# Optimization experiments

Hardware: AMD Instinct MI355X
Metric: run time of the kernel (lower is better)

The kernel has to match this reference:

```python
import jax, jax.numpy as jnp
import numpy as np

HIDDEN = 1024
HEADS = 16
HEAD_DIM = HIDDEN // HEADS
ROTARY_PCT = 0.25
ROTARY_DIM = int(HEAD_DIM * ROTARY_PCT)  # 16
BASE = 10000.0
SCALE = HEAD_DIM ** -0.5
EPS = 1e-8


def _rotate_half(x):
    h = x.shape[-1] // 2
    return jnp.concatenate([-x[..., h:], x[..., :h]], axis=-1)


def _apply_rope(q, k, position_ids):
    # q, k: [B, H, S, D]; NeoX-style partial rotary on first ROTARY_DIM dims
    inv_freq = 1.0 / (BASE ** (jnp.arange(0, ROTARY_DIM, 2, dtype=jnp.float32) / ROTARY_DIM))
    freqs = position_ids.astype(jnp.float32)[:, None] * inv_freq[None, :]  # [S, rd/2]
    emb = jnp.concatenate([freqs, freqs], axis=-1)  # [S, rd]
    cos = jnp.cos(emb)[None, None, :, :]
    sin = jnp.sin(emb)[None, None, :, :]

    def rot(x):
        x_rot, x_pass = x[..., :ROTARY_DIM], x[..., ROTARY_DIM:]
        x_rot = x_rot * cos + _rotate_half(x_rot) * sin
        return jnp.concatenate([x_rot, x_pass], axis=-1)

    return rot(q), rot(k)


def _ka_scan(attn_weights, value):
    # attn_weights: [B, H, S, S] causal softmax; value: [B, H, S, D]
    # A[0] = V[0]; A[i] = renorm(attn_weights[i, :i]) @ A[:i]
    S = value.shape[2]
    idx = jnp.arange(S)

    def step(a_buf, i):
        w = attn_weights[:, :, i, :]                      # [B, H, S]
        w = jnp.where(idx[None, None, :] < i, w, 0.0)     # strict past only
        w = w / (jnp.sum(w, axis=-1, keepdims=True) + EPS)
        a_i = jnp.einsum('bhs,bhsd->bhd', w, a_buf)
        a_i = jnp.where(i == 0, value[:, :, 0, :], a_i)
        a_buf = jax.lax.dynamic_update_slice(a_buf, a_i[:, :, None, :], (0, 0, i, 0))
        return a_buf, None

    a_buf, _ = jax.lax.scan(step, jnp.zeros_like(value), jnp.arange(S))
    return a_buf


def setup_inputs() -> dict:
    key = jax.random.key(0)
    k1, k2, k3 = jax.random.split(key, 3)
    B, S = 2, 2048
    hidden_states = jax.random.normal(k1, (B, S, HIDDEN), dtype=jnp.float32)
    position_ids = jnp.arange(S, dtype=jnp.int32)
    Wqkv = jax.random.normal(k2, (HIDDEN, 3 * HIDDEN), dtype=jnp.float32) / np.sqrt(HIDDEN)
    bqkv = jnp.zeros((3 * HIDDEN,), dtype=jnp.float32)
    Wd = jax.random.normal(k3, (HIDDEN, HIDDEN), dtype=jnp.float32) / np.sqrt(HIDDEN)
    bd = jnp.zeros((HIDDEN,), dtype=jnp.float32)
    return {"hidden_states": hidden_states, "position_ids": position_ids,
            "Wqkv": Wqkv, "bqkv": bqkv, "Wd": Wd, "bd": bd}


def reference(hidden_states, position_ids, Wqkv, bqkv, Wd, bd):
    B, S, _ = hidden_states.shape
    qkv = hidden_states @ Wqkv + bqkv                       # [B, S, 3*hidden]
    qkv = qkv.reshape(B, S, 3, HEADS, HEAD_DIM).transpose(2, 0, 3, 1, 4)
    query, key, value = qkv[0], qkv[1], qkv[2]              # [B, H, S, D]
    query, key = _apply_rope(query, key, position_ids)

    scores = jnp.einsum('bhqd,bhkd->bhqk', query, key) * SCALE
    causal = jnp.tril(jnp.ones((S, S), dtype=bool))
    scores = jnp.where(causal[None, None], scores, -jnp.inf)
    attn_weights = jax.nn.softmax(scores, axis=-1)          # [B, H, S, S]

    attn_output = _ka_scan(attn_weights, value)             # [B, H, S, D]
    attn_output = attn_output.transpose(0, 2, 1, 3).reshape(B, S, HIDDEN)
    return attn_output @ Wd + bd
```

## Files before the change

### kernel.cpp

```cpp
#include <hip/hip_runtime.h>

#define S_ 2048
#define EPSF 1e-8f
#define SCALEF 0.125f

typedef short bf16x8 __attribute__((ext_vector_type(8)));
typedef float f32x4 __attribute__((ext_vector_type(4)));

__device__ __forceinline__ unsigned short f2bf(float f){
  unsigned int u = __float_as_uint(f);
  u = (u + 0x7fffu + ((u >> 16) & 1u)) >> 16;
  return (unsigned short)u;
}
__device__ __forceinline__ float bf2f(unsigned short h){
  return __uint_as_float(((unsigned int)h) << 16);
}
__device__ __forceinline__ unsigned short f2bf_trunc(float f){
  return (unsigned short)(__float_as_uint(f) >> 16);
}

#define GLD16(g, l) __builtin_amdgcn_global_load_lds( \
    (const __attribute__((address_space(1))) unsigned int*)(g), \
    (__attribute__((address_space(3))) unsigned int*)(l), 16, 0, 0)

__global__ void k_prep(const float* __restrict__ hs, const float* __restrict__ Wqkv,
                       const float* __restrict__ bqkv, const float* __restrict__ Wd,
                       unsigned short* __restrict__ Ab,
                       unsigned short* __restrict__ WT,
                       float* __restrict__ U){
  __shared__ float t[32][33];
  __shared__ float red[4][64];
  __shared__ float vsh[64];
  int bid = blockIdx.x;
  if (bid < 4096){
    int i = (bid * 256 + threadIdx.x) * 4;
    float4 v = *(const float4*)(hs + i);
    ushort4 o; o.x=f2bf(v.x); o.y=f2bf(v.y); o.z=f2bf(v.z); o.w=f2bf(v.w);
    *(ushort4*)(Ab + i) = o;
  } else if (bid < 6144){
    int q = bid - 4096;
    int nt = q & 63, kt = q >> 6;
    int tx = threadIdx.x & 31, ty = threadIdx.x >> 5;
    #pragma unroll
    for (int r = 0; r < 32; r += 8)
      t[ty + r][tx] = Wqkv[(size_t)(kt*32 + ty + r)*3072 + nt*32 + tx];
    __syncthreads();
    #pragma unroll
    for (int r = 0; r < 32; r += 8)
      WT[(size_t)(nt*32 + ty + r)*1024 + kt*32 + tx] = f2bf(t[tx][ty + r]);
  } else {
    int bh = bid - 6144; int b = bh >> 4, h = bh & 15;
    int d = threadIdx.x & 63, kc = threadIdx.x >> 6;
    const float* x = hs + (size_t)b * S_ * 1024;
    int col = 2048 + h*64 + d;
    float acc = 0.f;
    #pragma unroll 8
    for (int k = kc*256; k < kc*256 + 256; ++k)
      acc = fmaf(x[k], Wqkv[(size_t)k*3072 + col], acc);
    red[kc][d] = acc;
    __syncthreads();
    if (kc == 0)
      vsh[d] = red[0][d] + red[1][d] + red[2][d] + red[3][d] + bqkv[col];
    __syncthreads();
    for (int n = threadIdx.x; n < 1024; n += 256){
      float a2 = 0.f;
      #pragma unroll 8
      for (int dd = 0; dd < 64; ++dd)
        a2 = fmaf(vsh[dd], Wd[(size_t)(h*64 + dd)*1024 + n], a2);
      U[(size_t)bh*1024 + n] = a2;
    }
  }
}

#define BK 32
__launch_bounds__(256)
__global__ void k_gemm_qk(const unsigned short* __restrict__ Ab,
                          const unsigned short* __restrict__ WT,
                          const float* __restrict__ bqkv,
                          const int* __restrict__ pos_ids,
                          unsigned short* __restrict__ Qb,
                          unsigned short* __restrict__ Kb){
  __shared__ unsigned short At[128*BK];
  __shared__ unsigned short Bt[128*BK];
  const int m0 = blockIdx.y * 128, n0 = blockIdx.x * 128;
  const int w = threadIdx.x >> 6, l = threadIdx.x & 63;
  const int wr = w >> 1, wc = w & 1;
  const int lq = l & 15, lh = l >> 4;
  f32x4 acc[4][4];
  #pragma unroll
  for (int i = 0; i < 4; ++i)
    #pragma unroll
    for (int j = 0; j < 4; ++j) acc[i][j] = (f32x4){0.f,0.f,0.f,0.f};

  const int srow = l >> 2;
  const int scol = (l & 3) * 8;

  for (int kt = 0; kt < 1024; kt += BK){
    GLD16(Ab + (size_t)(m0 + w*32 +      srow)*1024 + kt + scol, &At[(w*32)*BK]);
    GLD16(Ab + (size_t)(m0 + w*32 + 16 + srow)*1024 + kt + scol, &At[(w*32+16)*BK]);
    GLD16(WT + (size_t)(n0 + w*32 +      srow)*1024 + kt + scol, &Bt[(w*32)*BK]);
    GLD16(WT + (size_t)(n0 + w*32 + 16 + srow)*1024 + kt + scol, &Bt[(w*32+16)*BK]);
    __syncthreads();
    bf16x8 af[4], bf[4];
    #pragma unroll
    for (int i = 0; i < 4; ++i)
      af[i] = *(const bf16x8*)&At[(wr*64 + i*16 + lq)*BK + lh*8];
    #pragma unroll
    for (int j = 0; j < 4; ++j)
      bf[j] = *(const bf16x8*)&Bt[(wc*64 + j*16 + lq)*BK + lh*8];
    #pragma unroll
    for (int i = 0; i < 4; ++i)
      #pragma unroll
      for (int j = 0; j < 4; ++j)
        acc[i][j] = __builtin_amdgcn_mfma_f32_16x16x32_bf16(af[i], bf[j], acc[i][j], 0, 0, 0);
    __syncthreads();
  }
  #pragma unroll
  for (int i = 0; i < 4; ++i){
    #pragma unroll
    for (int j = 0; j < 4; ++j){
      #pragma unroll
      for (int r = 0; r < 4; ++r){
        int m = m0 + wr*64 + i*16 + (l>>4)*4 + r;
        int n = n0 + wc*64 + j*16 + (l&15);
        float v = acc[i][j][r] + bqkv[n];
        if (j == 0){
          float partner = __shfl_xor(v, 8);
          int s = m & 2047;
          float pos = (float)pos_ids[s];
          float fr = exp2f(-1.6609640474436813f * (float)(l & 7));
          float th = pos * fr;
          float sn = __sinf(th), cn = __cosf(th);
          v = ((l & 8) == 0) ? (v*cn - partner*sn) : (v*cn + partner*sn);
        }
        int b = m >> 11, s2 = m & 2047;
        int tsel = n >> 10; int nq = n & 1023;
        int h = nq >> 6, d = nq & 63;
        unsigned short* dst = tsel ? Kb : Qb;
        dst[((size_t)(b*16 + h)*S_ + s2)*64 + d] = f2bf(v);
      }
    }
  }
}

#define KST2 66
#define EST 68
__launch_bounds__(256, 4)
__global__ void k_scores(const unsigned short* __restrict__ Qb,
                         const unsigned short* __restrict__ Kb,
                         unsigned short* __restrict__ Eg,
                         float* __restrict__ rinvg){
  __shared__ unsigned short Ks[2][64*KST2];
  __shared__ unsigned short Es[4][16*EST];
  __shared__ float dsh[4][16];
  const int bi = blockIdx.x >> 5, bh = blockIdx.x & 31;
  const unsigned short* Qh = Qb + (size_t)bh * S_ * 64;
  const unsigned short* Kh = Kb + (size_t)bh * S_ * 64;
  const int tid = threadIdx.x, w = tid >> 6, l = tid & 63;
  const int lq = l & 15, lh = l >> 4;
  const unsigned short* qp = Qh + (size_t)(bi*64 + w*16 + lq)*64 + lh*8;
  bf16x8 qf0 = *(const bf16x8*)(qp);
  bf16x8 qf1 = *(const bf16x8*)(qp + 32);
  float dacc[4] = {0.f,0.f,0.f,0.f};
  unsigned short* Etile0 = Eg + ((size_t)bh*528 + (size_t)(bi*(bi+1)/2))*4096;
  const int srow = tid >> 2, sc = (tid & 3)*16;

  {
    const unsigned short* src = Kh + (size_t)srow*64 + sc;
    *(int4*)&Ks[0][srow*KST2 + sc]     = *(const int4*)(src);
    *(int4*)&Ks[0][srow*KST2 + sc + 8] = *(const int4*)(src + 8);
  }
  __syncthreads();

  for (int bj = 0; bj <= bi; ++bj){
    const int cur = bj & 1;
    int4 nk0, nk1;
    if (bj < bi){
      const unsigned short* src = Kh + (size_t)((bj+1)*64 + srow)*64 + sc;
      nk0 = *(const int4*)(src);
      nk1 = *(const int4*)(src + 8);
    }
    unsigned short* Et = Etile0 + (size_t)bj*4096 + w*1024;
    const bool diag = (bj == bi);
    #pragma unroll
    for (int ct = 0; ct < 4; ++ct){
      bf16x8 b0 = *(const bf16x8*)&Ks[cur][(ct*16 + lq)*KST2 + lh*8];
      bf16x8 b1 = *(const bf16x8*)&Ks[cur][(ct*16 + lq)*KST2 + 32 + lh*8];
      f32x4 a = (f32x4){0.f,0.f,0.f,0.f};
      a = __builtin_amdgcn_mfma_f32_16x16x32_bf16(qf0, b0, a, 0, 0, 0);
      a = __builtin_amdgcn_mfma_f32_16x16x32_bf16(qf1, b1, a, 0, 0, 0);
      #pragma unroll
      for (int r = 0; r < 4; ++r){
        float e = __expf(a[r] * SCALEF);
        unsigned short eb = f2bf_trunc(e);
        int rrow = lh*4 + r, col = ct*16 + lq;
        Es[w][rrow*EST + col] = eb;
        float ev = bf2f(eb);
        int grow = w*16 + rrow;
        if (!diag || col < grow) dacc[r] += ev;
        if (diag && col == grow) dsh[w][rrow] = ev;
      }
    }
    #pragma unroll
    for (int it = 0; it < 2; ++it){
      int row = it*8 + (l >> 3), eo = (l & 7)*8;
      *(int4*)(Et + row*64 + eo) = *(const int4*)&Es[w][row*EST + eo];
    }
    if (bj < bi){
      *(int4*)&Ks[cur^1][srow*KST2 + sc]     = nk0;
      *(int4*)&Ks[cur^1][srow*KST2 + sc + 8] = nk1;
    }
    __syncthreads();
  }
  #pragma unroll
  for (int r = 0; r < 4; ++r){
    float d = dacc[r];
    #pragma unroll
    for (int mm = 1; mm < 16; mm <<= 1) d += __shfl_xor(d, mm);
    float dE = dsh[w][lh*4 + r];
    float den = fmaf(EPSF, d + dE, d);
    float rv = 1.0f / den;
    if (lq == 0)
      rinvg[(size_t)bh*S_ + bi*64 + w*16 + lh*4 + r] = rv;
  }
}

__global__ __launch_bounds__(512)
__attribute__((amdgpu_waves_per_eu(2, 2)))
void k_recur3(const unsigned short* __restrict__ Eg,
              const float* __restrict__ rinvg,
              float* __restrict__ c_c,
              float* __restrict__ c_g){
  __shared__ float Pa[512];
  __shared__ float rso[512];
  __shared__ float csl[2][64];
  const int bh = blockIdx.x & 31, s = blockIdx.x >> 5;
  const unsigned short* Eh = Eg + (size_t)bh * 528 * 4096;
  const int tid = threadIdx.x, w = tid >> 6, l = tid & 63;
  const int lq = l & 15, lh = l >> 4;

  Pa[tid] = 0.f;
  rso[tid] = rinvg[(size_t)bh*S_ + (s + 4*w)*64 + l];
  __syncthreads();

  bf16x8 er[8];
  if (w == 0){
    const unsigned short* dt = Eh + ((size_t)(s*(s+1)/2) + s)*4096 + l*64;
    #pragma unroll
    for (int eb = 0; eb < 8; ++eb) er[eb] = *(const bf16x8*)(dt + eb*8);
  }

  bf16x8 dA0[5], dA1[5], dB0[5], dB1[5];
  bf16x8 ug0, ug1;
  const int lastc = s + 28;

  auto load_def = [&](int BJ, bf16x8 (&D0)[5], bf16x8 (&D1)[5]){
    int o0 = (BJ >= s) ? (((BJ - s) >> 2) + 1) : 0;
    int ex = (((BJ + 1) & 3) == s) ? 1 : 0;
    int nd = (8 - o0 - ex) * 4;
    if (w >= 1){
      #pragma unroll
      for (int k = 0; k < 5; ++k){
        int t = (w - 1) + k*7;
        if (t < nd){
          int ob = o0 + ex + (t >> 2);
          int bi = s + 4*ob;
          const unsigned short* tp =
              Eh + ((size_t)(bi*(bi+1)/2) + BJ)*4096 + (size_t)(t & 3)*1024;
          D0[k] = *(const bf16x8*)(tp + lq*64 + lh*8);
          D1[k] = *(const bf16x8*)(tp + lq*64 + 32 + lh*8);
        }
      }
      if (ex && w <= 4){
        int bi = BJ + 1;
        const unsigned short* tp =
            Eh + ((size_t)(bi*(bi+1)/2) + BJ)*4096 + (size_t)(w-1)*1024;
        ug0 = *(const bf16x8*)(tp + lq*64 + lh*8);
        ug1 = *(const bf16x8*)(tp + lq*64 + 32 + lh*8);
      }
    }
  };

  auto fold_def = [&](int BJP, bf16x8 (&D0)[5], bf16x8 (&D1)[5], int buf){
    int o0 = (BJP >= s) ? (((BJP - s) >> 2) + 1) : 0;
    int ex = (((BJP + 1) & 3) == s) ? 1 : 0;
    int nd = (8 - o0 - ex) * 4;
    if (w >= 1 && nd > 0){
      bf16x8 dc0 = (bf16x8){0,0,0,0,0,0,0,0};
      bf16x8 dc1 = (bf16x8){0,0,0,0,0,0,0,0};
      if (lq == 0){
        #pragma unroll
        for (int e = 0; e < 8; ++e){
          dc0[e] = (short)f2bf(csl[buf][lh*8 + e]);
          dc1[e] = (short)f2bf(csl[buf][32 + lh*8 + e]);
        }
      }
      #pragma unroll
      for (int k = 0; k < 5; ++k){
        int t = (w - 1) + k*7;
        if (t < nd){
          f32x4 o = (f32x4){0.f,0.f,0.f,0.f};
          o = __builtin_amdgcn_mfma_f32_16x16x32_bf16(D0[k], dc0, o, 0, 0, 0);
          o = __builtin_amdgcn_mfma_f32_16x16x32_bf16(D1[k], dc1, o, 0, 0, 0);
          if (lq == 0){
            int ob = o0 + ex + (t >> 2);
            float* base = Pa + ob*64 + (t & 3)*16 + lh*4;
            float4 v = *(float4*)base;
            v.x += o[0]; v.y += o[1]; v.z += o[2]; v.w += o[3];
            *(float4*)base = v;
          }
        }
      }
    }
  };

  auto iter = [&](int BJ, bf16x8 (&DL0)[5], bf16x8 (&DL1)[5],
                          bf16x8 (&DF0)[5], bf16x8 (&DF1)[5]){
    const int cur = BJ & 1;
    load_def(BJ, DL0, DL1);
    const int ex = (((BJ + 1) & 3) == s) ? 1 : 0;
    if (w == 0){
      if ((BJ & 3) == s){
        const int rr = l;
        const int o = (BJ - s) >> 2;
        float rinv = rso[o*64 + rr];
        float Pl = Pa[o*64 + rr];
        float cval = 0.f;
        #pragma unroll
        for (int eb = 0; eb < 8; ++eb){
          #pragma unroll
          for (int e = 0; e < 8; ++e){
            int r = eb*8 + e;
            float t2 = Pl * rinv;
            float cr = __uint_as_float(
                (unsigned)__builtin_amdgcn_readlane(__float_as_uint(t2), r));
            if (BJ == 0 && r == 0) cr = 1.0f;
            if (rr == r) cval = cr;
            float m = (rr > r) ? bf2f((unsigned short)er[eb][e]) : 0.f;
            Pl = fmaf(m, cr, Pl);
          }
        }
        csl[cur][rr] = cval;
        __hip_atomic_store((unsigned*)(c_c + (size_t)bh*S_ + BJ*64 + rr),
                           __float_as_uint(cval),
                           __ATOMIC_RELAXED, __HIP_MEMORY_SCOPE_AGENT);
        c_g[((size_t)(bh >> 4)*S_ + (BJ*64 + rr))*16 + (bh & 15)] = cval;
        int bn = BJ + 4;
        if (bn <= lastc){
          const unsigned short* dt =
              Eh + ((size_t)(bn*(bn+1)/2) + bn)*4096 + l*64;
          #pragma unroll
          for (int eb = 0; eb < 8; ++eb) er[eb] = *(const bf16x8*)(dt + eb*8);
        }
      } else {
        const unsigned* pp = (const unsigned*)(c_c + (size_t)bh*S_ + BJ*64 + l);
        unsigned v = __hip_atomic_load(pp, __ATOMIC_RELAXED,
                                       __HIP_MEMORY_SCOPE_AGENT);
        while (!__all(v != 0u)){
          __builtin_amdgcn_s_sleep(2);
          v = __hip_atomic_load(pp, __ATOMIC_RELAXED,
                                __HIP_MEMORY_SCOPE_AGENT);
        }
        csl[cur][l] = __uint_as_float(v);
      }
    } else if (BJ >= 1){
      fold_def(BJ - 1, DF0, DF1, cur ^ 1);
    }
    __syncthreads();
    if (ex && w >= 1 && w <= 4){
      bf16x8 uc0 = (bf16x8){0,0,0,0,0,0,0,0};
      bf16x8 uc1 = (bf16x8){0,0,0,0,0,0,0,0};
      if (lq == 0){
        #pragma unroll
        for (int e = 0; e < 8; ++e){
          uc0[e] = (short)f2bf(csl[cur][lh*8 + e]);
          uc1[e] = (short)f2bf(csl[cur][32 + lh*8 + e]);
        }
      }
      f32x4 o = (f32x4){0.f,0.f,0.f,0.f};
      o = __builtin_amdgcn_mfma_f32_16x16x32_bf16(ug0, uc0, o, 0, 0, 0);
      o = __builtin_amdgcn_mfma_f32_16x16x32_bf16(ug1, uc1, o, 0, 0, 0);
      if (lq == 0){
        int ou = (BJ + 1 - s) >> 2;
        float* base = Pa + ou*64 + (w-1)*16 + lh*4;
        float4 v = *(float4*)base;
        v.x += o[0]; v.y += o[1]; v.z += o[2]; v.w += o[3];
        *(float4*)base = v;
      }
    }
    __syncthreads();
  };

  for (int bj = 0; bj <= lastc; bj += 2){
    iter(bj,     dA0, dA1, dB0, dB1);
    if (bj + 1 <= lastc)
      iter(bj+1, dB0, dB1, dA0, dA1);
  }
}

__global__ void k_out(const float* __restrict__ c_g, const float* __restrict__ U,
                      const float* __restrict__ bd, float* __restrict__ out){
  int bs = blockIdx.x; int b = bs >> 11;
  __shared__ float ch[16];
  if (threadIdx.x < 16) ch[threadIdx.x] = c_g[(size_t)bs*16 + threadIdx.x];
  __syncthreads();
  int n = threadIdx.x * 4;
  float4 acc = *(const float4*)(bd + n);
  #pragma unroll
  for (int h = 0; h < 16; ++h){
    float cc = ch[h];
    float4 u = *(const float4*)(U + ((size_t)(b*16 + h))*1024 + n);
    acc.x = fmaf(cc, u.x, acc.x); acc.y = fmaf(cc, u.y, acc.y);
    acc.z = fmaf(cc, u.z, acc.z); acc.w = fmaf(cc, u.w, acc.w);
  }
  *(float4*)(out + (size_t)bs*1024 + n) = acc;
}

extern "C" void kernel_launch(void* const* d_in, const int* in_sizes, int n_in,
                              void* d_out, int out_size, void* d_ws, size_t ws_size,
                              hipStream_t stream) {
  const float* hs   = (const float*)d_in[0];
  const int*   pos  = (const int*)d_in[1];
  const float* Wqkv = (const float*)d_in[2];
  const float* bqkv = (const float*)d_in[3];
  const float* Wd   = (const float*)d_in[4];
  const float* bd   = (const float*)d_in[5];
  float* out = (float*)d_out;

  char* ws = (char*)d_ws;
  unsigned short* Ab = (unsigned short*)(ws);
  unsigned short* WT = (unsigned short*)(ws + (8u<<20));
  unsigned short* Qb = (unsigned short*)(ws + (12u<<20));
  unsigned short* Kb = (unsigned short*)(ws + (20u<<20));
  float* c_g  = (float*)(ws + (28u<<20) + 0x10000);
  float* U    = (float*)(ws + (28u<<20) + 0x50000);
  float* rinvg= (float*)(ws + (28u<<20) + 0x80000);
  float* c_c  = (float*)(ws + (28u<<20) + 0xC0000);
  unsigned short* Eg = (unsigned short*)(ws + (29u<<20));

  k_prep   <<<6176, 256, 0, stream>>>(hs, Wqkv, bqkv, Wd, Ab, WT, U);
  k_gemm_qk<<<dim3(16, 32), 256, 0, stream>>>(Ab, WT, bqkv, pos, Qb, Kb);
  k_scores <<<1024, 256, 0, stream>>>(Qb, Kb, Eg, rinvg);
  hipMemsetAsync(c_c, 0, 32 * S_ * sizeof(float), stream);
  k_recur3 <<<128, 512, 0, stream>>>(Eg, rinvg, c_c, c_g);
  k_out    <<<4096, 256, 0, stream>>>(c_g, U, bd, out);
}
```

Before: 201.8 us.

## Move urgent update MFMA into wave 0 and drop one barrier per iteration

The urgent-block update (ug loads plus MFMA) moves from waves 1-4 after a barrier into wave 0, which now loads all four 16-row tiles itself right after obtaining csl. This removes the second __syncthreads per iteration. Deferred folds and urgent updates can now touch the same Pa region concurrently, so the read-modify-write float4 updates become LDS atomicAdds. Deferred loads are issued after the fold instead of before. The cost is extra serial work on wave 0, which sits on the critical dependency chain, plus the overhead of the LDS atomics.

```diff
diff --git a/kernel.cpp b/kernel.cpp
--- a/kernel.cpp
+++ b/kernel.cpp
@@ -251,32 +251,22 @@
   }
 
   bf16x8 dA0[5], dA1[5], dB0[5], dB1[5];
-  bf16x8 ug0, ug1;
   const int lastc = s + 28;
 
   auto load_def = [&](int BJ, bf16x8 (&D0)[5], bf16x8 (&D1)[5]){
     int o0 = (BJ >= s) ? (((BJ - s) >> 2) + 1) : 0;
     int ex = (((BJ + 1) & 3) == s) ? 1 : 0;
     int nd = (8 - o0 - ex) * 4;
-    if (w >= 1){
-      #pragma unroll
-      for (int k = 0; k < 5; ++k){
-        int t = (w - 1) + k*7;
-        if (t < nd){
-          int ob = o0 + ex + (t >> 2);
-          int bi = s + 4*ob;
-          const unsigned short* tp =
-              Eh + ((size_t)(bi*(bi+1)/2) + BJ)*4096 + (size_t)(t & 3)*1024;
-          D0[k] = *(const bf16x8*)(tp + lq*64 + lh*8);
-          D1[k] = *(const bf16x8*)(tp + lq*64 + 32 + lh*8);
-        }
-      }
-      if (ex && w <= 4){
-        int bi = BJ + 1;
+    #pragma unroll
+    for (int k = 0; k < 5; ++k){
+      int t = (w - 1) + k*7;
+      if (t < nd){
+        int ob = o0 + ex + (t >> 2);
+        int bi = s + 4*ob;
         const unsigned short* tp =
-            Eh + ((size_t)(bi*(bi+1)/2) + BJ)*4096 + (size_t)(w-1)*1024;
-        ug0 = *(const bf16x8*)(tp + lq*64 + lh*8);
-        ug1 = *(const bf16x8*)(tp + lq*64 + 32 + lh*8);
+            Eh + ((size_t)(bi*(bi+1)/2) + BJ)*4096 + (size_t)(t & 3)*1024;
+        D0[k] = *(const bf16x8*)(tp + lq*64 + lh*8);
+        D1[k] = *(const bf16x8*)(tp + lq*64 + 32 + lh*8);
       }
     }
   };
@@ -285,7 +275,7 @@
     int o0 = (BJP >= s) ? (((BJP - s) >> 2) + 1) : 0;
     int ex = (((BJP + 1) & 3) == s) ? 1 : 0;
     int nd = (8 - o0 - ex) * 4;
-    if (w >= 1 && nd > 0){
+    if (nd > 0){
       bf16x8 dc0 = (bf16x8){0,0,0,0,0,0,0,0};
       bf16x8 dc1 = (bf16x8){0,0,0,0,0,0,0,0};
       if (lq == 0){
@@ -305,9 +295,10 @@
           if (lq == 0){
             int ob = o0 + ex + (t >> 2);
             float* base = Pa + ob*64 + (t & 3)*16 + lh*4;
-            float4 v = *(float4*)base;
-            v.x += o[0]; v.y += o[1]; v.z += o[2]; v.w += o[3];
-            *(float4*)base = v;
+            atomicAdd(base + 0, o[0]);
+            atomicAdd(base + 1, o[1]);
+            atomicAdd(base + 2, o[2]);
+            atomicAdd(base + 3, o[3]);
           }
         }
       }
@@ -317,9 +308,18 @@
   auto iter = [&](int BJ, bf16x8 (&DL0)[5], bf16x8 (&DL1)[5],
                           bf16x8 (&DF0)[5], bf16x8 (&DF1)[5]){
     const int cur = BJ & 1;
-    load_def(BJ, DL0, DL1);
     const int ex = (((BJ + 1) & 3) == s) ? 1 : 0;
     if (w == 0){
+      bf16x8 u0[4], u1[4];
+      if (ex){
+        int bi = BJ + 1;
+        const unsigned short* tp = Eh + ((size_t)(bi*(bi+1)/2) + BJ)*4096;
+        #pragma unroll
+        for (int q = 0; q < 4; ++q){
+          u0[q] = *(const bf16x8*)(tp + q*1024 + lq*64 + lh*8);
+          u1[q] = *(const bf16x8*)(tp + q*1024 + lq*64 + 32 + lh*8);
+        }
+      }
       if ((BJ & 3) == s){
         const int rr = l;
         const int o = (BJ - s) >> 2;
@@ -363,30 +363,34 @@
         }
         csl[cur][l] = __uint_as_float(v);
       }
-    } else if (BJ >= 1){
-      fold_def(BJ - 1, DF0, DF1, cur ^ 1);
-    }
-    __syncthreads();
-    if (ex && w >= 1 && w <= 4){
-      bf16x8 uc0 = (bf16x8){0,0,0,0,0,0,0,0};
-      bf16x8 uc1 = (bf16x8){0,0,0,0,0,0,0,0};
-      if (lq == 0){
+      if (ex){
+        bf16x8 uc0 = (bf16x8){0,0,0,0,0,0,0,0};
+        bf16x8 uc1 = (bf16x8){0,0,0,0,0,0,0,0};
+        if (lq == 0){
+          #pragma unroll
+          for (int e = 0; e < 8; ++e){
+            uc0[e] = (short)f2bf(csl[cur][lh*8 + e]);
+            uc1[e] = (short)f2bf(csl[cur][32 + lh*8 + e]);
+          }
+        }
+        const int ou = (BJ + 1 - s) >> 2;
         #pragma unroll
-        for (int e = 0; e < 8; ++e){
-          uc0[e] = (short)f2bf(csl[cur][lh*8 + e]);
-          uc1[e] = (short)f2bf(csl[cur][32 + lh*8 + e]);
-        }
-      }
-      f32x4 o = (f32x4){0.f,0.f,0.f,0.f};
-      o = __builtin_amdgcn_mfma_f32_16x16x32_bf16(ug0, uc0, o, 0, 0, 0);
-      o = __builtin_amdgcn_mfma_f32_16x16x32_bf16(ug1, uc1, o, 0, 0, 0);
-      if (lq == 0){
-        int ou = (BJ + 1 - s) >> 2;
-        float* base = Pa + ou*64 + (w-1)*16 + lh*4;
-        float4 v = *(float4*)base;
-        v.x += o[0]; v.y += o[1]; v.z += o[2]; v.w += o[3];
-        *(float4*)base = v;
-      }
+        for (int q = 0; q < 4; ++q){
+          f32x4 o = (f32x4){0.f,0.f,0.f,0.f};
+          o = __builtin_amdgcn_mfma_f32_16x16x32_bf16(u0[q], uc0, o, 0, 0, 0);
+          o = __builtin_amdgcn_mfma_f32_16x16x32_bf16(u1[q], uc1, o, 0, 0, 0);
+          if (lq == 0){
+            float* base = Pa + ou*64 + q*16 + lh*4;
+            atomicAdd(base + 0, o[0]);
+            atomicAdd(base + 1, o[1]);
+            atomicAdd(base + 2, o[2]);
+            atomicAdd(base + 3, o[3]);
+          }
+        }
+      }
+    } else {
+      if (BJ >= 1) fold_def(BJ - 1, DF0, DF1, cur ^ 1);
+      load_def(BJ, DL0, DL1);
     }
     __syncthreads();
   };
```

New measurement: 222.8 us. +10.4%, slower.

## Precompute inverse of diagonal triangular blocks to replace serial solve with MFMA

Applied to the files above, without the earlier changes.

A new kernel inverts each 64x64 unit-lower-triangular diagonal block of the recurrence (renormalised weights) ahead of time and stores it in bf16. The serial critical path in k_recur3 then applies the inverse with MFMA matrix-vector products instead of a 64-step readlane/FMA forward substitution. The c_c zeroing moves from hipMemsetAsync into k_prep. The aim is to shorten the serial dependency chain in the recurrence. The cost is an extra launch and bf16 rounding of the inverse and of the right-hand side, which may reduce accuracy.

```diff
diff --git a/kernel.cpp b/kernel.cpp
--- a/kernel.cpp
+++ b/kernel.cpp
@@ -27,7 +27,8 @@
                        const float* __restrict__ bqkv, const float* __restrict__ Wd,
                        unsigned short* __restrict__ Ab,
                        unsigned short* __restrict__ WT,
-                       float* __restrict__ U){
+                       float* __restrict__ U,
+                       float* __restrict__ c_c){
   __shared__ float t[32][33];
   __shared__ float red[4][64];
   __shared__ float vsh[64];
@@ -48,7 +49,7 @@
     #pragma unroll
     for (int r = 0; r < 32; r += 8)
       WT[(size_t)(nt*32 + ty + r)*1024 + kt*32 + tx] = f2bf(t[tx][ty + r]);
-  } else {
+  } else if (bid < 6176){
     int bh = bid - 6144; int b = bh >> 4, h = bh & 15;
     int d = threadIdx.x & 63, kc = threadIdx.x >> 6;
     const float* x = hs + (size_t)b * S_ * 1024;
@@ -69,6 +70,10 @@
         a2 = fmaf(vsh[dd], Wd[(size_t)(h*64 + dd)*1024 + n], a2);
       U[(size_t)bh*1024 + n] = a2;
     }
+  } else {
+    int q = bid - 6176;
+    float4 z = (float4){0.f,0.f,0.f,0.f};
+    *(float4*)(c_c + (size_t)q*1024 + threadIdx.x*4) = z;
   }
 }
 
@@ -225,15 +230,47 @@
   }
 }
 
+__global__ __launch_bounds__(64)
+void k_dinv(const unsigned short* __restrict__ Eg,
+            const float* __restrict__ rinvg,
+            unsigned short* __restrict__ Dg){
+  __shared__ float As[64*65];
+  const int bh = blockIdx.x >> 5, bi = blockIdx.x & 31;
+  const unsigned short* Et =
+      Eg + ((size_t)bh*528 + (size_t)(bi*(bi+1)/2) + bi)*4096;
+  const int c = threadIdx.x;
+  for (int r = 0; r < 64; ++r){
+    float rv = rinvg[(size_t)bh*S_ + bi*64 + r];
+    float e = bf2f(Et[(r>>4)*1024 + (r&15)*64 + c]);
+    As[r*65 + c] = (c < r) ? e * rv : 0.f;
+  }
+  __syncthreads();
+  float X[64];
+  #pragma unroll
+  for (int r = 0; r < 64; ++r){
+    float acc = (r == c) ? 1.f : 0.f;
+    #pragma unroll
+    for (int k = 0; k < r; ++k)
+      acc = fmaf(As[r*65 + k], X[k], acc);
+    X[r] = acc;
+  }
+  unsigned short* dt = Dg + (size_t)blockIdx.x * 4096;
+  #pragma unroll
+  for (int r = 0; r < 64; ++r)
+    dt[(r>>4)*1024 + (r&15)*64 + c] = f2bf(X[r]);
+}
+
 __global__ __launch_bounds__(512)
 __attribute__((amdgpu_waves_per_eu(2, 2)))
 void k_recur3(const unsigned short* __restrict__ Eg,
+              const unsigned short* __restrict__ Dg,
               const float* __restrict__ rinvg,
               float* __restrict__ c_c,
               float* __restrict__ c_g){
   __shared__ float Pa[512];
   __shared__ float rso[512];
   __shared__ float csl[2][64];
+  __shared__ float bb[64];
   const int bh = blockIdx.x & 31, s = blockIdx.x >> 5;
   const unsigned short* Eh = Eg + (size_t)bh * 528 * 4096;
   const int tid = threadIdx.x, w = tid >> 6, l = tid & 63;
@@ -243,11 +280,14 @@
   rso[tid] = rinvg[(size_t)bh*S_ + (s + 4*w)*64 + l];
   __syncthreads();
 
-  bf16x8 er[8];
+  bf16x8 dv0[4], dv1[4];
   if (w == 0){
-    const unsigned short* dt = Eh + ((size_t)(s*(s+1)/2) + s)*4096 + l*64;
-    #pragma unroll
-    for (int eb = 0; eb < 8; ++eb) er[eb] = *(const bf16x8*)(dt + eb*8);
+    const unsigned short* dt = Dg + (size_t)(bh*32 + s)*4096;
+    #pragma unroll
+    for (int q = 0; q < 4; ++q){
+      dv0[q] = *(const bf16x8*)(dt + q*1024 + lq*64 + lh*8);
+      dv1[q] = *(const bf16x8*)(dt + q*1024 + lq*64 + 32 + lh*8);
+    }
   }
 
   bf16x8 dA0[5], dA1[5], dB0[5], dB1[5];
@@ -321,36 +361,43 @@
     const int ex = (((BJ + 1) & 3) == s) ? 1 : 0;
     if (w == 0){
       if ((BJ & 3) == s){
-        const int rr = l;
         const int o = (BJ - s) >> 2;
-        float rinv = rso[o*64 + rr];
-        float Pl = Pa[o*64 + rr];
-        float cval = 0.f;
-        #pragma unroll
-        for (int eb = 0; eb < 8; ++eb){
+        float bval = rso[o*64 + l] * Pa[o*64 + l];
+        if (BJ == 0 && l == 0) bval = 1.0f;
+        bb[l] = bval;
+        bf16x8 uc0 = (bf16x8){0,0,0,0,0,0,0,0};
+        bf16x8 uc1 = (bf16x8){0,0,0,0,0,0,0,0};
+        if (lq == 0){
           #pragma unroll
           for (int e = 0; e < 8; ++e){
-            int r = eb*8 + e;
-            float t2 = Pl * rinv;
-            float cr = __uint_as_float(
-                (unsigned)__builtin_amdgcn_readlane(__float_as_uint(t2), r));
-            if (BJ == 0 && r == 0) cr = 1.0f;
-            if (rr == r) cval = cr;
-            float m = (rr > r) ? bf2f((unsigned short)er[eb][e]) : 0.f;
-            Pl = fmaf(m, cr, Pl);
+            uc0[e] = (short)f2bf(bb[lh*8 + e]);
+            uc1[e] = (short)f2bf(bb[32 + lh*8 + e]);
           }
         }
-        csl[cur][rr] = cval;
-        __hip_atomic_store((unsigned*)(c_c + (size_t)bh*S_ + BJ*64 + rr),
+        #pragma unroll
+        for (int q = 0; q < 4; ++q){
+          f32x4 o4 = (f32x4){0.f,0.f,0.f,0.f};
+          o4 = __builtin_amdgcn_mfma_f32_16x16x32_bf16(dv0[q], uc0, o4, 0, 0, 0);
+          o4 = __builtin_amdgcn_mfma_f32_16x16x32_bf16(dv1[q], uc1, o4, 0, 0, 0);
+          if (lq == 0){
+            #pragma unroll
+            for (int r = 0; r < 4; ++r)
+              csl[cur][q*16 + lh*4 + r] = o4[r];
+          }
+        }
+        float cval = csl[cur][l];
+        __hip_atomic_store((unsigned*)(c_c + (size_t)bh*S_ + BJ*64 + l),
                            __float_as_uint(cval),
                            __ATOMIC_RELAXED, __HIP_MEMORY_SCOPE_AGENT);
-        c_g[((size_t)(bh >> 4)*S_ + (BJ*64 + rr))*16 + (bh & 15)] = cval;
+        c_g[((size_t)(bh >> 4)*S_ + (BJ*64 + l))*16 + (bh & 15)] = cval;
         int bn = BJ + 4;
         if (bn <= lastc){
-          const unsigned short* dt =
-              Eh + ((size_t)(bn*(bn+1)/2) + bn)*4096 + l*64;
+          const unsigned short* dt = Dg + (size_t)(bh*32 + bn)*4096;
           #pragma unroll
-          for (int eb = 0; eb < 8; ++eb) er[eb] = *(const bf16x8*)(dt + eb*8);
+          for (int q = 0; q < 4; ++q){
+            dv0[q] = *(const bf16x8*)(dt + q*1024 + lq*64 + lh*8);
+            dv1[q] = *(const bf16x8*)(dt + q*1024 + lq*64 + 32 + lh*8);
+          }
         }
       } else {
         const unsigned* pp = (const unsigned*)(c_c + (size_t)bh*S_ + BJ*64 + l);
@@ -429,6 +476,7 @@
 
   char* ws = (char*)d_ws;
   unsigned short* Ab = (unsigned short*)(ws);
+  unsigned short* Dg = (unsigned short*)(ws);
   unsigned short* WT = (unsigned short*)(ws + (8u<<20));
   unsigned short* Qb = (unsigned short*)(ws + (12u<<20));
   unsigned short* Kb = (unsigned short*)(ws + (20u<<20));
@@ -438,10 +486,10 @@
   float* c_c  = (float*)(ws + (28u<<20) + 0xC0000);
   unsigned short* Eg = (unsigned short*)(ws + (29u<<20));
 
-  k_prep   <<<6176, 256, 0, stream>>>(hs, Wqkv, bqkv, Wd, Ab, WT, U);
+  k_prep   <<<6240, 256, 0, stream>>>(hs, Wqkv, bqkv, Wd, Ab, WT, U, c_c);
   k_gemm_qk<<<dim3(16, 32), 256, 0, stream>>>(Ab, WT, bqkv, pos, Qb, Kb);
   k_scores <<<1024, 256, 0, stream>>>(Qb, Kb, Eg, rinvg);
-  hipMemsetAsync(c_c, 0, 32 * S_ * sizeof(float), stream);
-  k_recur3 <<<128, 512, 0, stream>>>(Eg, rinvg, c_c, c_g);
+  k_dinv   <<<1024, 64, 0, stream>>>(Eg, rinvg, Dg);
+  k_recur3 <<<128, 512, 0, stream>>>(Eg, Dg, rinvg, c_c, c_g);
   k_out    <<<4096, 256, 0, stream>>>(c_g, U, bd, out);
 }
```

Measured after the change: 201.7 us. No clear change (-0.1%).
